# Performance work log

Hardware: AMD Instinct MI355X
Metric: run time of the kernel (lower is better)

The kernel has to match this reference:

```python
import jax, jax.numpy as jnp
import numpy as np

LN_EPS = 1e-5

def layernorm(x, w, b):
    mu = jnp.mean(x, axis=-1, keepdims=True)
    var = jnp.mean(jnp.square(x - mu), axis=-1, keepdims=True)
    return (x - mu) * jax.lax.rsqrt(var + LN_EPS) * w + b

def l2_normalize(x, eps=1e-12):
    n = jnp.sqrt(jnp.sum(jnp.square(x), axis=-1, keepdims=True))
    return x / jnp.maximum(n, eps)

def setup_inputs() -> dict:
    key = jax.random.key(0)
    k1, k2 = jax.random.split(key)
    B, D, Npix = 8, 64, 32768
    K, P = 19, 5
    return {
        "base_feature": jax.random.normal(k1, (B, D, Npix), dtype=jnp.float32),
        "means": jax.random.normal(k2, (K, P, D), dtype=jnp.float32) * 0.02,  # trunc_normal_(std=0.02)
        "diagonal": jnp.ones((K, P, D), dtype=jnp.float32),
        "feat_w": jnp.ones((D,), dtype=jnp.float32),
        "feat_b": jnp.zeros((D,), dtype=jnp.float32),
        "mask_w": jnp.ones((K,), dtype=jnp.float32),
        "mask_b": jnp.zeros((K,), dtype=jnp.float32),
    }

def gmm_log_prob(x, mu, scale):
    # x: [N, D]; mu, scale: [KP, D]  (MultivariateNormalDiag with scale_diag=scale)
    # log p = -0.5 * sum(((x-mu)/s)^2) - sum(log s) - 0.5*D*log(2*pi)
    D = x.shape[-1]
    inv2 = 1.0 / jnp.square(scale)                      # [KP, D]
    quad = (jnp.square(x) @ inv2.T                       # [N, KP]
            - 2.0 * (x @ (mu * inv2).T)
            + jnp.sum(jnp.square(mu) * inv2, axis=-1))
    log_norm = jnp.sum(jnp.log(scale), axis=-1) + 0.5 * D * jnp.log(2.0 * jnp.pi)
    return -0.5 * quad - log_norm                        # [N, KP]

def reference(base_feature, means, diagonal, feat_w, feat_b, mask_w, mask_b):
    B, D, Npix = base_feature.shape
    K, P, _ = means.shape
    # 'b c n -> (b n) c'
    _c = jnp.transpose(base_feature, (0, 2, 1)).reshape(B * Npix, D)
    _c = layernorm(_c, feat_w, feat_b)
    _c = l2_normalize(_c)
    means_n = l2_normalize(means)                        # means.data.copy_(l2_normalize(means))
    logp = gmm_log_prob(_c, means_n.reshape(K * P, D), diagonal.reshape(K * P, D))
    final_probs = logp.reshape(-1, K, P)                 # [(b n), K, P]
    _m_prob = jnp.max(final_probs, axis=-1)              # amax over components -> [(b n), K]
    out_seg = layernorm(_m_prob, mask_w, mask_b)         # mask_norm
    # '(b n) k -> b k n'
    out_seg = jnp.transpose(out_seg.reshape(B, Npix, K), (0, 2, 1))
    return out_seg
```

## Files before the change

### kernel.cpp

```cpp
#include <hip/hip_runtime.h>
#include <math.h>

#define BB    8
#define DD    64
#define NPIX  32768
#define KK    19
#define PP    5
#define NROW  112

#define XDW   2048
#define AOFF  8192
#define ADW   68
#define COFF  15808

typedef _Float16 half8  __attribute__((ext_vector_type(8)));
typedef __fp16   half2t __attribute__((ext_vector_type(2)));
typedef float    f32x4  __attribute__((ext_vector_type(4)));

union H8 { half8 v; half2t p[4]; };

__global__ __launch_bounds__(64) void gmm_prep(
        const float* __restrict__ means, const float* __restrict__ diag,
        const float* __restrict__ feat_w, const float* __restrict__ feat_b,
        _Float16* __restrict__ Ch, float* __restrict__ cst,
        float* __restrict__ scal) {
    const int R = blockIdx.x;
    const int d = threadIdx.x;
    if (R == NROW) {
        float w = feat_w[d], b = feat_b[d];
        float s0 = w * w, s1 = w * b, s2 = b * b;
        #pragma unroll
        for (int off = 32; off; off >>= 1) {
            s0 += __shfl_xor(s0, off);
            s1 += __shfl_xor(s1, off);
            s2 += __shfl_xor(s2, off);
        }
        if (d == 0) { scal[0] = s0; scal[1] = s1; scal[2] = s2; }
        return;
    }
    int g, p; bool valid;
    if (R < 80)      { g = 4 * (R >> 4) + ((R >> 2) & 3); p = R & 3; valid = (g < KK); }
    else if (R < 96) { g = 4 * ((R - 80) & 3) + ((R - 80) >> 2); p = 4; valid = true; }
    else             { g = 16 + ((R - 96) >> 2); p = 4; valid = ((R & 3) == 0) && (g < KK); }
    if (valid) {
        const int j = 5 * g + p;
        float mu = means[j * DD + d];
        float sc = diag[j * DD + d];
        float ss = mu * mu;
        #pragma unroll
        for (int off = 32; off; off >>= 1) ss += __shfl_xor(ss, off);
        float inv = 1.f / fmaxf(sqrtf(ss), 1e-12f);
        float mn = mu * inv;
        float i2 = 1.f / (sc * sc);
        Ch[R * 128 + 2 * d]     = (_Float16)(mn * i2);
        Ch[R * 128 + 2 * d + 1] = (_Float16)(-0.5f * i2);
        float c1 = mn * mn * i2;
        float c2 = logf(sc);
        #pragma unroll
        for (int off = 32; off; off >>= 1) {
            c1 += __shfl_xor(c1, off);
            c2 += __shfl_xor(c2, off);
        }
        if (d == 0) cst[R] = -0.5f * c1 - c2;
    } else {
        Ch[R * 128 + 2 * d]     = (_Float16)0.f;
        Ch[R * 128 + 2 * d + 1] = (_Float16)0.f;
        if (d == 0) cst[R] = 0.f;
    }
}

__global__ __launch_bounds__(256, 2) void gmm_main(
        const float* __restrict__ bf,
        const float* __restrict__ feat_w, const float* __restrict__ feat_b,
        const float* __restrict__ mask_w, const float* __restrict__ mask_b,
        const _Float16* __restrict__ Ch, const float* __restrict__ cst,
        const float* __restrict__ scal, float* __restrict__ out) {
    __shared__ __align__(16) float smem[15920];

    const int tid  = threadIdx.x;
    const int w    = tid >> 6;
    const int lane = tid & 63;
    const int m15  = lane & 15;
    const int q    = lane >> 4;
    const int bidx = blockIdx.x;
    const int b    = bidx >> 8;
    const int n0   = ((bidx & 255) << 7) + (w << 5);
    float* lp = smem + w * XDW;

    const int rr  = lane >> 3;
    const int c4  = (lane & 7) * 4;
    const float* xg = bf + (size_t)b * (DD * NPIX) + n0 + c4;
    float4 xv[8];
    #pragma unroll
    for (int j = 0; j < 8; ++j)
        xv[j] = *(const float4*)(xg + (size_t)(8 * j + rr) * NPIX);

    {
        const float4* Cg = (const float4*)Ch;
        #pragma unroll
        for (int it = 0; it < 7; ++it) {
            const int f = it * 256 + tid;
            const float4 v = Cg[f];
            *(float4*)(smem + AOFF + (f >> 4) * ADW + (f & 15) * 4) = v;
        }
        if (tid < NROW) smem[COFF + tid] = cst[tid];
    }

    float4 wv[4], bv[4];
    #pragma unroll
    for (int ks = 0; ks < 4; ++ks) {
        wv[ks] = *(const float4*)(feat_w + ks * 16 + q * 4);
        bv[ks] = *(const float4*)(feat_b + ks * 16 + q * 4);
    }

    #pragma unroll
    for (int j = 0; j < 8; ++j) {
        const int row = 8 * j + rr;
        *(float4*)(lp + row * 32 + (c4 ^ (rr << 2))) = xv[j];
    }

    __syncthreads();

    float xs0[16], xs1[16];
    #pragma unroll
    for (int ks = 0; ks < 4; ++ks)
        #pragma unroll
        for (int i = 0; i < 4; ++i) {
            const int row = 16 * ks + 4 * q + i;
            const int sw  = (row & 7) << 2;
            xs0[ks * 4 + i] = lp[row * 32 + (m15 ^ sw)];
            xs1[ks * 4 + i] = lp[row * 32 + ((m15 + 16) ^ sw)];
        }

    float S1a = 0.f, S2a = 0.f, S3a = 0.f, S4a = 0.f, S5a = 0.f;
    float S1b = 0.f, S2b = 0.f, S3b = 0.f, S4b = 0.f, S5b = 0.f;
    #pragma unroll
    for (int ks = 0; ks < 4; ++ks)
        #pragma unroll
        for (int i = 0; i < 4; ++i) {
            float wd = ((const float*)&wv[ks])[i];
            float bd = ((const float*)&bv[ks])[i];
            float xa = xs0[ks * 4 + i], xb = xs1[ks * 4 + i];
            float ta = wd * xa, tb = wd * xb;
            S1a += xa; S2a = fmaf(xa, xa, S2a); S3a = fmaf(ta, ta, S3a);
            S4a = fmaf(ta, wd, S4a); S5a = fmaf(ta, bd, S5a);
            S1b += xb; S2b = fmaf(xb, xb, S2b); S3b = fmaf(tb, tb, S3b);
            S4b = fmaf(tb, wd, S4b); S5b = fmaf(tb, bd, S5b);
        }
    S1a += __shfl_xor(S1a, 16); S1a += __shfl_xor(S1a, 32);
    S2a += __shfl_xor(S2a, 16); S2a += __shfl_xor(S2a, 32);
    S3a += __shfl_xor(S3a, 16); S3a += __shfl_xor(S3a, 32);
    S4a += __shfl_xor(S4a, 16); S4a += __shfl_xor(S4a, 32);
    S5a += __shfl_xor(S5a, 16); S5a += __shfl_xor(S5a, 32);
    S1b += __shfl_xor(S1b, 16); S1b += __shfl_xor(S1b, 32);
    S2b += __shfl_xor(S2b, 16); S2b += __shfl_xor(S2b, 32);
    S3b += __shfl_xor(S3b, 16); S3b += __shfl_xor(S3b, 32);
    S4b += __shfl_xor(S4b, 16); S4b += __shfl_xor(S4b, 32);
    S5b += __shfl_xor(S5b, 16); S5b += __shfl_xor(S5b, 32);

    const float W2 = scal[0], WB = scal[1], B2 = scal[2];
    float al0, e0, f0, al1, e1, f1;
    {
        float mu  = S1a * (1.f / 64.f);
        float var = fmaxf(S2a * (1.f / 64.f) - mu * mu, 0.f);
        float r   = rsqrtf(var + 1e-5f);
        float Sy2 = r * r * (S3a - 2.f * mu * S4a + mu * mu * W2)
                  + 2.f * r * (S5a - mu * WB) + B2;
        float invn = 1.f / fmaxf(sqrtf(fmaxf(Sy2, 0.f)), 1e-12f);
        al0 = invn * r; e0 = invn; f0 = -al0 * mu;
    }
    {
        float mu  = S1b * (1.f / 64.f);
        float var = fmaxf(S2b * (1.f / 64.f) - mu * mu, 0.f);
        float r   = rsqrtf(var + 1e-5f);
        float Sy2 = r * r * (S3b - 2.f * mu * S4b + mu * mu * W2)
                  + 2.f * r * (S5b - mu * WB) + B2;
        float invn = 1.f / fmaxf(sqrtf(fmaxf(Sy2, 0.f)), 1e-12f);
        al1 = invn * r; e1 = invn; f1 = -al1 * mu;
    }

    H8 Uh[2][4], Ul[2][4];
    #pragma unroll
    for (int ks = 0; ks < 4; ++ks) {
        #pragma unroll
        for (int i = 0; i < 4; ++i) {
            float wd = ((const float*)&wv[ks])[i];
            float bd = ((const float*)&bv[ks])[i];
            float c0 = fmaf(f0, wd, e0 * bd);
            float c1 = fmaf(f1, wd, e1 * bd);
            float u0 = fmaf(al0, wd * xs0[ks * 4 + i], c0);
            float u1 = fmaf(al1, wd * xs1[ks * 4 + i], c1);
            float q0 = u0 * u0, q1 = u1 * u1;
            half2t h0 = __builtin_amdgcn_cvt_pkrtz(u0, q0);
            half2t h1 = __builtin_amdgcn_cvt_pkrtz(u1, q1);
            half2t l0 = __builtin_amdgcn_cvt_pkrtz(u0 - (float)h0[0], q0 - (float)h0[1]);
            half2t l1 = __builtin_amdgcn_cvt_pkrtz(u1 - (float)h1[0], q1 - (float)h1[1]);
            Uh[0][ks].p[i] = h0; Ul[0][ks].p[i] = l0;
            Uh[1][ks].p[i] = h1; Ul[1][ks].p[i] = l1;
        }
    }

    const char* Ab = (const char*)(smem + AOFF) + (size_t)m15 * 272 + q * 16;
    float m0[5], m1[5];
    #pragma unroll
    for (int t = 0; t < 7; ++t) {
        half8 Ac[4];
        #pragma unroll
        for (int ks = 0; ks < 4; ++ks)
            Ac[ks] = *(const half8*)(Ab + (size_t)t * 16 * 272 + ks * 64);
        const float4 cv = *(const float4*)(smem + COFF + 16 * t + 4 * q);
        f32x4 a0 = {0.f, 0.f, 0.f, 0.f}, a1 = {0.f, 0.f, 0.f, 0.f};
        #pragma unroll
        for (int ks = 0; ks < 4; ++ks) {
            a0 = __builtin_amdgcn_mfma_f32_16x16x32_f16(Ac[ks], Uh[0][ks].v, a0, 0, 0, 0);
            a1 = __builtin_amdgcn_mfma_f32_16x16x32_f16(Ac[ks], Uh[1][ks].v, a1, 0, 0, 0);
        }
        #pragma unroll
        for (int ks = 0; ks < 4; ++ks) {
            a0 = __builtin_amdgcn_mfma_f32_16x16x32_f16(Ac[ks], Ul[0][ks].v, a0, 0, 0, 0);
            a1 = __builtin_amdgcn_mfma_f32_16x16x32_f16(Ac[ks], Ul[1][ks].v, a1, 0, 0, 0);
        }
        if (t < 5) {
            m0[t] = fmaxf(fmaxf(a0[0] + cv.x, a0[1] + cv.y), fmaxf(a0[2] + cv.z, a0[3] + cv.w));
            m1[t] = fmaxf(fmaxf(a1[0] + cv.x, a1[1] + cv.y), fmaxf(a1[2] + cv.z, a1[3] + cv.w));
        } else if (t == 5) {
            m0[0] = fmaxf(m0[0], a0[0] + cv.x);
            m0[1] = fmaxf(m0[1], a0[1] + cv.y);
            m0[2] = fmaxf(m0[2], a0[2] + cv.z);
            m0[3] = fmaxf(m0[3], a0[3] + cv.w);
            m1[0] = fmaxf(m1[0], a1[0] + cv.x);
            m1[1] = fmaxf(m1[1], a1[1] + cv.y);
            m1[2] = fmaxf(m1[2], a1[2] + cv.z);
            m1[3] = fmaxf(m1[3], a1[3] + cv.w);
        } else {
            m0[4] = fmaxf(m0[4], a0[0] + cv.x);
            m1[4] = fmaxf(m1[4], a1[0] + cv.x);
        }
    }

    const bool v4 = (q < 3);
    float S0 = m0[0] + m0[1] + m0[2] + m0[3] + (v4 ? m0[4] : 0.f);
    float S1 = m1[0] + m1[1] + m1[2] + m1[3] + (v4 ? m1[4] : 0.f);
    S0 += __shfl_xor(S0, 16); S0 += __shfl_xor(S0, 32);
    S1 += __shfl_xor(S1, 16); S1 += __shfl_xor(S1, 32);
    const float mu0 = S0 * (1.f / 19.f), mu1 = S1 * (1.f / 19.f);
    float V0, V1;
    {
        float d0 = m0[0] - mu0, d1 = m0[1] - mu0, d2 = m0[2] - mu0;
        float d3 = m0[3] - mu0, d4 = m0[4] - mu0;
        V0 = d0 * d0 + d1 * d1 + d2 * d2 + d3 * d3 + (v4 ? d4 * d4 : 0.f);
    }
    {
        float d0 = m1[0] - mu1, d1 = m1[1] - mu1, d2 = m1[2] - mu1;
        float d3 = m1[3] - mu1, d4 = m1[4] - mu1;
        V1 = d0 * d0 + d1 * d1 + d2 * d2 + d3 * d3 + (v4 ? d4 * d4 : 0.f);
    }
    V0 += __shfl_xor(V0, 16); V0 += __shfl_xor(V0, 32);
    V1 += __shfl_xor(V1, 16); V1 += __shfl_xor(V1, 32);
    const float r0 = rsqrtf(V0 * (1.f / 19.f) + 1e-5f);
    const float r1 = rsqrtf(V1 * (1.f / 19.f) + 1e-5f);

    __syncthreads();

    #pragma unroll
    for (int t = 0; t < 5; ++t) {
        const int k = 4 * t + q;
        if (t < 4 || v4) {
            const float mw = mask_w[k], mb = mask_b[k];
            lp[k * 32 + m15]      = (m0[t] - mu0) * r0 * mw + mb;
            lp[k * 32 + 16 + m15] = (m1[t] - mu1) * r1 * mw + mb;
        }
    }

    __syncthreads();

    float* ob = out + (size_t)b * (KK * NPIX) + n0;
    #pragma unroll
    for (int rnd = 0; rnd < 3; ++rnd) {
        const int idx = rnd * 64 + lane;
        if (idx < 152) {
            const int k = idx >> 3, cc = (idx & 7) * 4;
            float4 v = *(const float4*)(lp + k * 32 + cc);
            *(float4*)(ob + (size_t)k * NPIX + cc) = v;
        }
    }
}

extern "C" void kernel_launch(void* const* d_in, const int* in_sizes, int n_in,
                              void* d_out, int out_size, void* d_ws, size_t ws_size,
                              hipStream_t stream) {
    const float* base_feature = (const float*)d_in[0];
    const float* means        = (const float*)d_in[1];
    const float* diagonal     = (const float*)d_in[2];
    const float* feat_w       = (const float*)d_in[3];
    const float* feat_b       = (const float*)d_in[4];
    const float* mask_w       = (const float*)d_in[5];
    const float* mask_b       = (const float*)d_in[6];
    float* out = (float*)d_out;

    _Float16* Ch = (_Float16*)d_ws;
    float* cst   = (float*)(Ch + NROW * 128);
    float* scal  = cst + NROW;

    gmm_prep<<<NROW + 1, 64, 0, stream>>>(means, diagonal, feat_w, feat_b, Ch, cst, scal);

    gmm_main<<<(BB * NPIX) / 128, 256, 0, stream>>>(
        base_feature, feat_w, feat_b, mask_w, mask_b, Ch, cst, scal, out);
}
```

Before: 124.2 us.

## Load tiles directly to LDS and alias coefficient buffer over input tile

Input feature tiles and the fp16 coefficient matrix are now loaded straight into LDS with global_load_lds, skipping the trip through registers. The coefficient matrix reuses the LDS region of the input tile after it has been read into registers, using an XOR swizzle instead of padding. This cuts shared memory per block enough to raise launch bounds to three blocks per CU, aiming for more occupancy and latency hiding. The cost is two extra block barriers and the coefficient load now starts only after the input tile has been consumed.

After: 122.4 us, median of 3. About the same (-1.4%).

```diff
diff --git a/kernel.cpp b/kernel.cpp
--- a/kernel.cpp
+++ b/kernel.cpp
@@ -8,16 +8,20 @@
 #define PP    5
 #define NROW  112
 
-#define XDW   2048
-#define AOFF  8192
-#define ADW   68
-#define COFF  15808
+#define XDW    2048
+#define CSTOFF 8192
 
 typedef _Float16 half8  __attribute__((ext_vector_type(8)));
 typedef __fp16   half2t __attribute__((ext_vector_type(2)));
 typedef float    f32x4  __attribute__((ext_vector_type(4)));
 
 union H8 { half8 v; half2t p[4]; };
+
+__device__ __forceinline__ void gload16(const void* g, void* l) {
+    __builtin_amdgcn_global_load_lds(
+        (const __attribute__((address_space(1))) void*)g,
+        (__attribute__((address_space(3))) void*)l, 16, 0, 0);
+}
 
 __global__ __launch_bounds__(64) void gmm_prep(
         const float* __restrict__ means, const float* __restrict__ diag,
@@ -69,13 +73,13 @@
     }
 }
 
-__global__ __launch_bounds__(256, 2) void gmm_main(
+__global__ __launch_bounds__(256, 3) void gmm_main(
         const float* __restrict__ bf,
         const float* __restrict__ feat_w, const float* __restrict__ feat_b,
         const float* __restrict__ mask_w, const float* __restrict__ mask_b,
         const _Float16* __restrict__ Ch, const float* __restrict__ cst,
         const float* __restrict__ scal, float* __restrict__ out) {
-    __shared__ __align__(16) float smem[15920];
+    __shared__ __align__(16) float smem[8304];
 
     const int tid  = threadIdx.x;
     const int w    = tid >> 6;
@@ -88,23 +92,13 @@
     float* lp = smem + w * XDW;
 
     const int rr  = lane >> 3;
-    const int c4  = (lane & 7) * 4;
-    const float* xg = bf + (size_t)b * (DD * NPIX) + n0 + c4;
-    float4 xv[8];
+    const int c4s = ((lane & 7) * 4) ^ (rr << 2);
+    const float* xgb = bf + (size_t)b * (DD * NPIX) + n0;
     #pragma unroll
     for (int j = 0; j < 8; ++j)
-        xv[j] = *(const float4*)(xg + (size_t)(8 * j + rr) * NPIX);
-
-    {
-        const float4* Cg = (const float4*)Ch;
-        #pragma unroll
-        for (int it = 0; it < 7; ++it) {
-            const int f = it * 256 + tid;
-            const float4 v = Cg[f];
-            *(float4*)(smem + AOFF + (f >> 4) * ADW + (f & 15) * 4) = v;
-        }
-        if (tid < NROW) smem[COFF + tid] = cst[tid];
-    }
+        gload16(xgb + (size_t)(8 * j + rr) * NPIX + c4s, lp + 8 * j * 32);
+
+    if (tid < NROW) smem[CSTOFF + tid] = cst[tid];
 
     float4 wv[4], bv[4];
     #pragma unroll
@@ -112,12 +106,7 @@
         wv[ks] = *(const float4*)(feat_w + ks * 16 + q * 4);
         bv[ks] = *(const float4*)(feat_b + ks * 16 + q * 4);
     }
-
-    #pragma unroll
-    for (int j = 0; j < 8; ++j) {
-        const int row = 8 * j + rr;
-        *(float4*)(lp + row * 32 + (c4 ^ (rr << 2))) = xv[j];
-    }
+    const float W2 = scal[0], WB = scal[1], B2 = scal[2];
 
     __syncthreads();
 
@@ -131,6 +120,19 @@
             xs0[ks * 4 + i] = lp[row * 32 + (m15 ^ sw)];
             xs1[ks * 4 + i] = lp[row * 32 + ((m15 + 16) ^ sw)];
         }
+
+    __syncthreads();
+
+    {
+        const char* Cg = (const char*)Ch;
+        #pragma unroll
+        for (int i = 0; i < 7; ++i) {
+            const int f   = (w * 7 + i) * 64 + lane;
+            const int row = f >> 4, ch = f & 15;
+            gload16(Cg + (size_t)row * 256 + ((ch ^ (row & 15)) * 16),
+                    smem + (size_t)(w * 7 + i) * 256);
+        }
+    }
 
     float S1a = 0.f, S2a = 0.f, S3a = 0.f, S4a = 0.f, S5a = 0.f;
     float S1b = 0.f, S2b = 0.f, S3b = 0.f, S4b = 0.f, S5b = 0.f;
@@ -158,7 +160,6 @@
     S4b += __shfl_xor(S4b, 16); S4b += __shfl_xor(S4b, 32);
     S5b += __shfl_xor(S5b, 16); S5b += __shfl_xor(S5b, 32);
 
-    const float W2 = scal[0], WB = scal[1], B2 = scal[2];
     float al0, e0, f0, al1, e1, f1;
     {
         float mu  = S1a * (1.f / 64.f);
@@ -200,15 +201,17 @@
         }
     }
 
-    const char* Ab = (const char*)(smem + AOFF) + (size_t)m15 * 272 + q * 16;
+    __syncthreads();
+
     float m0[5], m1[5];
     #pragma unroll
     for (int t = 0; t < 7; ++t) {
         half8 Ac[4];
         #pragma unroll
         for (int ks = 0; ks < 4; ++ks)
-            Ac[ks] = *(const half8*)(Ab + (size_t)t * 16 * 272 + ks * 64);
-        const float4 cv = *(const float4*)(smem + COFF + 16 * t + 4 * q);
+            Ac[ks] = *(const half8*)((const char*)smem
+                        + (size_t)(16 * t + m15) * 256 + (((ks * 4 + q) ^ m15) * 16));
+        const float4 cv = *(const float4*)(smem + CSTOFF + 16 * t + 4 * q);
         f32x4 a0 = {0.f, 0.f, 0.f, 0.f}, a1 = {0.f, 0.f, 0.f, 0.f};
         #pragma unroll
         for (int ks = 0; ks < 4; ++ks) {
```
